# Optimization experiments

Hardware: AMD Instinct MI355X
Metric: run time of the kernel (lower is better)

## Reference

```python
import jax, jax.numpy as jnp
import numpy as np

EPS = 1e-9  # Dice BatchNorm epsilon

def _dice(x, alpha, mm, mv):
    # Keras BN(center=False, scale=False) in inference mode: (x - moving_mean) / sqrt(moving_var + eps)
    p = jax.nn.sigmoid((x - mm) * jax.lax.rsqrt(mv + EPS))
    return x * (p + alpha * (1.0 - p))

def setup_inputs() -> dict:
    key = jax.random.key(0)
    ks = jax.random.split(key, 8)
    B, T, E = 4096, 200, 12
    return {
        "query": jax.random.normal(ks[0], (B, 1, E), jnp.float32),
        "keys": jax.random.normal(ks[1], (B, T, E), jnp.float32),
        "mask": jnp.ones((B, T), dtype=bool),
        "W0": jax.random.normal(ks[2], (48, 80), jnp.float32) * (1.0 / np.sqrt(48)),
        "b0": jnp.zeros((80,), jnp.float32),
        "W1": jax.random.normal(ks[3], (80, 40), jnp.float32) * (1.0 / np.sqrt(80)),
        "b1": jnp.zeros((40,), jnp.float32),
        "alpha0": jax.random.uniform(ks[4], (80,), jnp.float32),
        "alpha1": jax.random.uniform(ks[5], (40,), jnp.float32),
        "mm0": jnp.zeros((80,), jnp.float32),
        "mv0": jnp.ones((80,), jnp.float32),
        "mm1": jnp.zeros((40,), jnp.float32),
        "mv1": jnp.ones((40,), jnp.float32),
        "atten_kernel": jax.random.normal(ks[6], (40, 1), jnp.float32) * (1.0 / np.sqrt(40)),
        "atten_bias": jnp.zeros((1,), jnp.float32),
    }

def reference(query, keys, mask, W0, b0, W1, b1, alpha0, alpha1,
              mm0, mv0, mm1, mv1, atten_kernel, atten_bias):
    B, T, E = keys.shape
    q = jnp.broadcast_to(query, (B, T, E))  # K.repeat_elements(query, T, 1)
    att = jnp.concatenate([q, keys, q - keys, q * keys], axis=-1)  # [B, T, 4E=48]
    h = _dice(jnp.einsum('bti,io->bto', att, W0) + b0, alpha0, mm0, mv0)  # [B,T,80]
    h = _dice(jnp.einsum('bti,io->bto', h, W1) + b1, alpha1, mm1, mv1)    # [B,T,40]
    score = jnp.einsum('bti,io->bto', h, atten_kernel) + atten_bias       # [B,T,1]
    scores = jnp.swapaxes(score, 1, 2)  # [B,1,T]
    # NOTE: original code computes tf.where(mask,...) but overwrites it and
    # matmuls the UNMASKED scores with keys (bug reproduced faithfully).
    return jnp.matmul(scores, keys)  # [B,1,E]
```

## Files before the change

### kernel.cpp

```cpp
#include <hip/hip_runtime.h>
#include <math.h>

#define B_TOT 4096
#define T_LEN 200
#define E_DIM 12
#define LOG2E 1.44269504088896340736f

typedef __attribute__((ext_vector_type(8))) short bf16x8;
typedef __attribute__((ext_vector_type(4))) float f32x4;


__device__ inline unsigned short f2bf(float f) {
    union { float f; unsigned u; } x; x.f = f;
    unsigned r = x.u + 0x7FFFu + ((x.u >> 16) & 1u);
    return (unsigned short)(r >> 16);
}

__global__ __launch_bounds__(256) void din_prep(
    const float* __restrict__ W0, const float* __restrict__ b0v,
    const float* __restrict__ W1, const float* __restrict__ b1v,
    const float* __restrict__ a0, const float* __restrict__ a1,
    const float* __restrict__ mm0, const float* __restrict__ mv0,
    const float* __restrict__ mm1, const float* __restrict__ mv1,
    const float* __restrict__ ak, void* __restrict__ wsv)
{
    unsigned char* wsb = (unsigned char*)wsv;
    unsigned short* w0e = (unsigned short*)wsb;
    unsigned short* w1e = (unsigned short*)(wsb + 10240);
    float* d0c = (float*)(wsb + 19456);
    float* d1c = (float*)(wsb + 20736);

    int idx = blockIdx.x * 256 + threadIdx.x;
    if (idx < 5120) {
        int n = idx >> 6, k = idx & 63;
        float v;
        if (k < 12)        v = W0[(12 + k) * 80 + n] - W0[(24 + k) * 80 + n];
        else if (k < 24)   v = W0[(36 + (k - 12)) * 80 + n];
        else if (k < 36)   v = W0[(k - 24) * 80 + n] + W0[(24 + (k - 24)) * 80 + n];
        else if (k == 36)  v = b0v[n];
        else               v = 0.0f;
        w0e[n * 64 + k] = f2bf(v);
    } else if (idx < 9728) {
        int v2 = idx - 5120;
        int n = v2 / 96, k = v2 - n * 96;
        float v = 0.0f;
        if (n < 40) {
            if (k < 80)       v = W1[k * 40 + n];
            else if (k == 80) v = b1v[n];
        }
        w1e[n * 96 + k] = f2bf(v);
    } else if (idx < 10048) {
        int v2 = idx - 9728;
        int o = v2 >> 2, c = v2 & 3;
        float rs = rsqrtf(mv0[o] + 1e-9f) * LOG2E;
        float val = (c == 0) ? -rs : (c == 1) ? mm0[o] * rs : (c == 2) ? a0[o] : 1.0f - a0[o];
        d0c[o * 4 + c] = val;
    } else {
        int v2 = idx - 10048;
        int j = v2 >> 2, c = v2 & 3;
        float val = 0.0f;
        if (j < 40) {
            float rs = rsqrtf(mv1[j] + 1e-9f) * LOG2E;
            val = (c == 0) ? -rs : (c == 1) ? mm1[j] * rs : (c == 2) ? a1[j] * ak[j]
                                                          : (1.0f - a1[j]) * ak[j];
        }
        d1c[j * 4 + c] = val;
    }
}

#define A0_STRIDE 72
#define H_STRIDE  104

__global__ __launch_bounds__(256, 2) void din_mfma(
    const float* __restrict__ query, const float* __restrict__ keys,
    const float* __restrict__ abias_p, const void* __restrict__ wsv,
    float* __restrict__ out)
{
    __shared__ __align__(16) unsigned short Aseg[4 * 64];
    __shared__ __align__(16) unsigned short A0[4 * 64 * A0_STRIDE];
    __shared__ __align__(16) unsigned short H[4 * 16 * H_STRIDE];

    const unsigned char* wsb = (const unsigned char*)wsv;
    const unsigned short* w0e = (const unsigned short*)wsb;
    const unsigned short* w1e = (const unsigned short*)(wsb + 10240);
    const f32x4* d0cp = (const f32x4*)(wsb + 19456);
    const f32x4* d1cp = (const f32x4*)(wsb + 20736);

    const int tid = threadIdx.x;
    const int lane = tid & 63;
    const int w = tid >> 6;
    const int l15 = lane & 15;
    const int quad = lane >> 4;
    const int b = blockIdx.x * 4 + w;

    unsigned short* A0w = &A0[w * 64 * A0_STRIDE];
    unsigned short* Hw  = &H[w * 16 * H_STRIDE];
    unsigned short* Asw = &Aseg[w * 64];

    bf16x8 b0f[5][2];
    #pragma unroll
    for (int nt = 0; nt < 5; ++nt)
        #pragma unroll
        for (int ks = 0; ks < 2; ++ks)
            b0f[nt][ks] = *(const bf16x8*)(w0e + (nt * 16 + l15) * 64 + ks * 32 + quad * 8);
    bf16x8 b1f[3][3];
    #pragma unroll
    for (int nt = 0; nt < 3; ++nt)
        #pragma unroll
        for (int ks = 0; ks < 3; ++ks)
            b1f[nt][ks] = *(const bf16x8*)(w1e + (nt * 16 + l15) * 96 + ks * 32 + quad * 8);
    f32x4 d0c[5];
    #pragma unroll
    for (int nt = 0; nt < 5; ++nt) d0c[nt] = d0cp[nt * 16 + l15];
    f32x4 d1c[3];
    #pragma unroll
    for (int nt = 0; nt < 3; ++nt) d1c[nt] = d1cp[nt * 16 + l15];
    const float abias = abias_p[0];

    float qq[12];
    {
        const float4* qp = (const float4*)(query + (size_t)b * E_DIM);
        float4 q0 = qp[0], q1 = qp[1], q2 = qp[2];
        qq[0]=q0.x; qq[1]=q0.y; qq[2]=q0.z; qq[3]=q0.w;
        qq[4]=q1.x; qq[5]=q1.y; qq[6]=q1.z; qq[7]=q1.w;
        qq[8]=q2.x; qq[9]=q2.y; qq[10]=q2.z; qq[11]=q2.w;
    }
    unsigned qqw[6];
    #pragma unroll
    for (int i = 0; i < 6; ++i)
        qqw[i] = (unsigned)f2bf(qq[2 * i]) | ((unsigned)f2bf(qq[2 * i + 1]) << 16);

    if (quad == 0) {
        bf16x8 one8 = {(short)0x3F80, 0, 0, 0, 0, 0, 0, 0};
        bf16x8 zero8 = {0, 0, 0, 0, 0, 0, 0, 0};
        *(bf16x8*)(Hw + l15 * H_STRIDE + 80) = one8;
        *(bf16x8*)(Hw + l15 * H_STRIDE + 88) = zero8;
    }

    f32x4 acc2 = {0.f, 0.f, 0.f, 0.f};

    for (int c = 0; c < 4; ++c) {
        const int t0 = c * 64;
        const int myT = t0 + lane;
        const bool valid = myT < T_LEN;

        float kk[12];
        if (valid) {
            const float4* kp = (const float4*)(keys + ((size_t)b * T_LEN + myT) * E_DIM);
            float4 k0 = kp[0], k1 = kp[1], k2 = kp[2];
            kk[0]=k0.x; kk[1]=k0.y; kk[2]=k0.z; kk[3]=k0.w;
            kk[4]=k1.x; kk[5]=k1.y; kk[6]=k1.z; kk[7]=k1.w;
            kk[8]=k2.x; kk[9]=k2.y; kk[10]=k2.z; kk[11]=k2.w;
        } else {
            #pragma unroll
            for (int i = 0; i < 12; ++i) kk[i] = 0.0f;
        }
        {
            unsigned wds[32];
            #pragma unroll
            for (int i = 0; i < 6; ++i)
                wds[i] = (unsigned)f2bf(kk[2 * i]) | ((unsigned)f2bf(kk[2 * i + 1]) << 16);
            #pragma unroll
            for (int i = 0; i < 6; ++i)
                wds[6 + i] = (unsigned)f2bf(qq[2 * i] * kk[2 * i])
                           | ((unsigned)f2bf(qq[2 * i + 1] * kk[2 * i + 1]) << 16);
            #pragma unroll
            for (int i = 0; i < 6; ++i) wds[12 + i] = qqw[i];
            wds[18] = 0x00003F80u;
            #pragma unroll
            for (int i = 19; i < 32; ++i) wds[i] = 0u;
            unsigned short* dst = A0w + lane * A0_STRIDE;
            #pragma unroll
            for (int v = 0; v < 8; ++v) {
                bf16x8 pk;
                #pragma unroll
                for (int h = 0; h < 4; ++h) {
                    unsigned u = wds[v * 4 + h];
                    pk[2 * h]     = (short)(u & 0xFFFF);
                    pk[2 * h + 1] = (short)(u >> 16);
                }
                *(bf16x8*)(dst + v * 8) = pk;
            }
        }
        Asw[lane] = 0;

        const int ntiles = (c < 3) ? 4 : 1;
        for (int ti = 0; ti < ntiles; ++ti) {
            const unsigned short* ar = A0w + (ti * 16 + l15) * A0_STRIDE + quad * 8;
            bf16x8 a0 = *(const bf16x8*)ar;
            bf16x8 a1 = *(const bf16x8*)(ar + 32);

            f32x4 acc[5];
            #pragma unroll
            for (int nt = 0; nt < 5; ++nt) {
                f32x4 cc = {0.f, 0.f, 0.f, 0.f};
                cc = __builtin_amdgcn_mfma_f32_16x16x32_bf16(a0, b0f[nt][0], cc, 0, 0, 0);
                cc = __builtin_amdgcn_mfma_f32_16x16x32_bf16(a1, b0f[nt][1], cc, 0, 0, 0);
                acc[nt] = cc;
            }
            #pragma unroll
            for (int nt = 0; nt < 5; ++nt) {
                #pragma unroll
                for (int r = 0; r < 4; ++r) {
                    float z = acc[nt][r];
                    float pg = __builtin_amdgcn_rcpf(
                        1.0f + __builtin_amdgcn_exp2f(fmaf(z, d0c[nt].x, d0c[nt].y)));
                    float h = z * fmaf(pg, d0c[nt].w, d0c[nt].z);
                    Hw[(quad * 4 + r) * H_STRIDE + nt * 16 + l15] = f2bf(h);
                }
            }
            bf16x8 af[3];
            #pragma unroll
            for (int ks = 0; ks < 3; ++ks)
                af[ks] = *(const bf16x8*)(Hw + l15 * H_STRIDE + ks * 32 + quad * 8);
            float s[4] = {0.f, 0.f, 0.f, 0.f};
            #pragma unroll
            for (int nt = 0; nt < 3; ++nt) {
                f32x4 cc = {0.f, 0.f, 0.f, 0.f};
                #pragma unroll
                for (int ks = 0; ks < 3; ++ks)
                    cc = __builtin_amdgcn_mfma_f32_16x16x32_bf16(af[ks], b1f[nt][ks], cc, 0, 0, 0);
                #pragma unroll
                for (int r = 0; r < 4; ++r) {
                    float z = cc[r];
                    float pg = __builtin_amdgcn_rcpf(
                        1.0f + __builtin_amdgcn_exp2f(fmaf(z, d1c[nt].x, d1c[nt].y)));
                    s[r] = fmaf(z, fmaf(pg, d1c[nt].w, d1c[nt].z), s[r]);
                }
            }
            #pragma unroll
            for (int m = 1; m < 16; m <<= 1) {
                #pragma unroll
                for (int r = 0; r < 4; ++r) s[r] += __shfl_xor(s[r], m, 64);
            }
            if (l15 == 0) {
                unsigned long long pk = 0ull;
                #pragma unroll
                for (int r = 0; r < 4; ++r) {
                    int t = t0 + ti * 16 + quad * 4 + r;
                    unsigned short sb = (t < T_LEN) ? f2bf(s[r] + abias) : (unsigned short)0;
                    pk |= (unsigned long long)sb << (16 * r);
                }
                *(unsigned long long*)(Asw + ti * 16 + quad * 4) = pk;
            }
        }

        #pragma unroll
        for (int ks = 0; ks < 2; ++ks) {
            bf16x8 pa = *(const bf16x8*)(Asw + l15 * 64 + ks * 32 + quad * 8);
            bf16x8 bk;
            #pragma unroll
            for (int j = 0; j < 8; ++j)
                bk[j] = (short)A0w[(ks * 32 + quad * 8 + j) * A0_STRIDE + l15];
            acc2 = __builtin_amdgcn_mfma_f32_16x16x32_bf16(pa, bk, acc2, 0, 0, 0);
        }
    }

    if (quad == 0 && l15 < 12)
        out[(size_t)b * E_DIM + l15] = acc2[0];
}

extern "C" void kernel_launch(void* const* d_in, const int* in_sizes, int n_in,
                              void* d_out, int out_size, void* d_ws, size_t ws_size,
                              hipStream_t stream) {
    const float* query = (const float*)d_in[0];
    const float* keys  = (const float*)d_in[1];
    const float* W0  = (const float*)d_in[3];
    const float* b0v = (const float*)d_in[4];
    const float* W1  = (const float*)d_in[5];
    const float* b1v = (const float*)d_in[6];
    const float* a0  = (const float*)d_in[7];
    const float* a1  = (const float*)d_in[8];
    const float* mm0 = (const float*)d_in[9];
    const float* mv0 = (const float*)d_in[10];
    const float* mm1 = (const float*)d_in[11];
    const float* mv1 = (const float*)d_in[12];
    const float* ak  = (const float*)d_in[13];
    const float* ab  = (const float*)d_in[14];
    float* out = (float*)d_out;

    hipLaunchKernelGGL(din_prep, dim3(40), dim3(256), 0, stream,
                       W0, b0v, W1, b1v, a0, a1, mm0, mv0, mm1, mv1, ak, d_ws);
    hipLaunchKernelGGL(din_mfma, dim3(B_TOT / 4), dim3(256), 0, stream,
                       query, keys, ab, d_ws, out);
}
```

Baseline: 155.9 us.

## Hoist per-batch query terms out of layer-0 GEMM and raise occupancy

The query-only part of the first layer (q·(W0a+W0c) plus bias) is computed once per batch row with one MFMA per output tile and added as a per-column offset. This halves the K dimension of the per-token layer-0 GEMM from 64 to 32 and shrinks the A0 LDS tile. W1 fragments and Dice constants are now reloaded from global/cache inside the loop rather than held in registers, and launch bounds move to 4 blocks per CU for higher occupancy. The trade is more memory traffic for weights against fewer VGPRs and MFMAs.

```diff
diff --git a/kernel.cpp b/kernel.cpp
--- a/kernel.cpp
+++ b/kernel.cpp
@@ -1,4 +1,5 @@
 #include <hip/hip_runtime.h>
+#include <hip/hip_bf16.h>
 #include <math.h>
 
 #define B_TOT 4096
@@ -8,12 +9,19 @@
 
 typedef __attribute__((ext_vector_type(8))) short bf16x8;
 typedef __attribute__((ext_vector_type(4))) float f32x4;
+typedef unsigned short ushort_t;
 
 
 __device__ inline unsigned short f2bf(float f) {
     union { float f; unsigned u; } x; x.f = f;
     unsigned r = x.u + 0x7FFFu + ((x.u >> 16) & 1u);
     return (unsigned short)(r >> 16);
+}
+__device__ inline unsigned pk_bf16(float a, float b) {
+    float2 t; t.x = a; t.y = b;
+    __hip_bfloat162 h = __float22bfloat162_rn(t);
+    union { __hip_bfloat162 h; unsigned u; } cv; cv.h = h;
+    return cv.u;
 }
 
 __global__ __launch_bounds__(256) void din_prep(
@@ -25,21 +33,26 @@
     const float* __restrict__ ak, void* __restrict__ wsv)
 {
     unsigned char* wsb = (unsigned char*)wsv;
-    unsigned short* w0e = (unsigned short*)wsb;
-    unsigned short* w1e = (unsigned short*)(wsb + 10240);
+    ushort_t* w0e2 = (ushort_t*)wsb;
+    ushort_t* wq   = (ushort_t*)(wsb + 5120);
+    ushort_t* w1e  = (ushort_t*)(wsb + 10240);
     float* d0c = (float*)(wsb + 19456);
     float* d1c = (float*)(wsb + 20736);
 
     int idx = blockIdx.x * 256 + threadIdx.x;
-    if (idx < 5120) {
-        int n = idx >> 6, k = idx & 63;
-        float v;
-        if (k < 12)        v = W0[(12 + k) * 80 + n] - W0[(24 + k) * 80 + n];
-        else if (k < 24)   v = W0[(36 + (k - 12)) * 80 + n];
-        else if (k < 36)   v = W0[(k - 24) * 80 + n] + W0[(24 + (k - 24)) * 80 + n];
-        else if (k == 36)  v = b0v[n];
-        else               v = 0.0f;
-        w0e[n * 64 + k] = f2bf(v);
+    if (idx < 2560) {
+        int n = idx >> 5, k = idx & 31;
+        float v = 0.0f;
+        if (k < 12)       v = W0[(12 + k) * 80 + n] - W0[(24 + k) * 80 + n];
+        else if (k < 24)  v = W0[(36 + (k - 12)) * 80 + n];
+        w0e2[n * 32 + k] = f2bf(v);
+    } else if (idx < 5120) {
+        int v2 = idx - 2560;
+        int n = v2 >> 5, k = v2 & 31;
+        float v = 0.0f;
+        if (k < 12)       v = W0[k * 80 + n] + W0[(24 + k) * 80 + n];
+        else if (k == 12) v = b0v[n];
+        wq[n * 32 + k] = f2bf(v);
     } else if (idx < 9728) {
         int v2 = idx - 5120;
         int n = v2 / 96, k = v2 - n * 96;
@@ -68,21 +81,21 @@
     }
 }
 
-#define A0_STRIDE 72
-#define H_STRIDE  104
-
-__global__ __launch_bounds__(256, 2) void din_mfma(
+#define A0_STR 40
+#define H_STR  104
+
+__global__ __launch_bounds__(256, 4) void din_mfma(
     const float* __restrict__ query, const float* __restrict__ keys,
     const float* __restrict__ abias_p, const void* __restrict__ wsv,
     float* __restrict__ out)
 {
-    __shared__ __align__(16) unsigned short Aseg[4 * 64];
-    __shared__ __align__(16) unsigned short A0[4 * 64 * A0_STRIDE];
-    __shared__ __align__(16) unsigned short H[4 * 16 * H_STRIDE];
-
+    __shared__ __align__(16) ushort_t Aseg[4 * 64];
+    __shared__ __align__(16) ushort_t A0[4 * 64 * A0_STR];
+    __shared__ __align__(16) ushort_t H[4 * 16 * H_STR];
     const unsigned char* wsb = (const unsigned char*)wsv;
-    const unsigned short* w0e = (const unsigned short*)wsb;
-    const unsigned short* w1e = (const unsigned short*)(wsb + 10240);
+    const ushort_t* w0e2 = (const ushort_t*)wsb;
+    const ushort_t* wq   = (const ushort_t*)(wsb + 5120);
+    const ushort_t* w1e  = (const ushort_t*)(wsb + 10240);
     const f32x4* d0cp = (const f32x4*)(wsb + 19456);
     const f32x4* d1cp = (const f32x4*)(wsb + 20736);
 
@@ -93,29 +106,14 @@
     const int quad = lane >> 4;
     const int b = blockIdx.x * 4 + w;
 
-    unsigned short* A0w = &A0[w * 64 * A0_STRIDE];
-    unsigned short* Hw  = &H[w * 16 * H_STRIDE];
-    unsigned short* Asw = &Aseg[w * 64];
-
-    bf16x8 b0f[5][2];
+    ushort_t* A0w = &A0[w * 64 * A0_STR];
+    ushort_t* Hw  = &H[w * 16 * H_STR];
+    ushort_t* Asw = &Aseg[w * 64];
+
+    bf16x8 b0f[5];
     #pragma unroll
     for (int nt = 0; nt < 5; ++nt)
-        #pragma unroll
-        for (int ks = 0; ks < 2; ++ks)
-            b0f[nt][ks] = *(const bf16x8*)(w0e + (nt * 16 + l15) * 64 + ks * 32 + quad * 8);
-    bf16x8 b1f[3][3];
-    #pragma unroll
-    for (int nt = 0; nt < 3; ++nt)
-        #pragma unroll
-        for (int ks = 0; ks < 3; ++ks)
-            b1f[nt][ks] = *(const bf16x8*)(w1e + (nt * 16 + l15) * 96 + ks * 32 + quad * 8);
-    f32x4 d0c[5];
-    #pragma unroll
-    for (int nt = 0; nt < 5; ++nt) d0c[nt] = d0cp[nt * 16 + l15];
-    f32x4 d1c[3];
-    #pragma unroll
-    for (int nt = 0; nt < 3; ++nt) d1c[nt] = d1cp[nt * 16 + l15];
-    const float abias = abias_p[0];
+        b0f[nt] = *(const bf16x8*)(w0e2 + (nt * 16 + l15) * 32 + quad * 8);
 
     float qq[12];
     {
@@ -125,16 +123,34 @@
         qq[4]=q1.x; qq[5]=q1.y; qq[6]=q1.z; qq[7]=q1.w;
         qq[8]=q2.x; qq[9]=q2.y; qq[10]=q2.z; qq[11]=q2.w;
     }
-    unsigned qqw[6];
-    #pragma unroll
-    for (int i = 0; i < 6; ++i)
-        qqw[i] = (unsigned)f2bf(qq[2 * i]) | ((unsigned)f2bf(qq[2 * i + 1]) << 16);
+
+    float z0q[5];
+    {
+        unsigned dw0, dw1, dw2, dw3;
+        unsigned p01 = pk_bf16(qq[0], qq[1]), p23 = pk_bf16(qq[2], qq[3]);
+        unsigned p45 = pk_bf16(qq[4], qq[5]), p67 = pk_bf16(qq[6], qq[7]);
+        unsigned p89 = pk_bf16(qq[8], qq[9]), pab = pk_bf16(qq[10], qq[11]);
+        dw0 = (quad == 0) ? p01 : (quad == 1) ? p89 : 0u;
+        dw1 = (quad == 0) ? p23 : (quad == 1) ? pab : 0u;
+        dw2 = (quad == 0) ? p45 : (quad == 1) ? 0x00003F80u : 0u;
+        dw3 = (quad == 0) ? p67 : 0u;
+        union { unsigned u[4]; bf16x8 v; } qa;
+        qa.u[0] = dw0; qa.u[1] = dw1; qa.u[2] = dw2; qa.u[3] = dw3;
+        #pragma unroll
+        for (int nt = 0; nt < 5; ++nt) {
+            bf16x8 wf = *(const bf16x8*)(wq + (nt * 16 + l15) * 32 + quad * 8);
+            f32x4 zz = {0.f, 0.f, 0.f, 0.f};
+            zz = __builtin_amdgcn_mfma_f32_16x16x32_bf16(qa.v, wf, zz, 0, 0, 0);
+            z0q[nt] = zz[0];
+        }
+    }
+    const float abias = abias_p[0];
 
     if (quad == 0) {
         bf16x8 one8 = {(short)0x3F80, 0, 0, 0, 0, 0, 0, 0};
         bf16x8 zero8 = {0, 0, 0, 0, 0, 0, 0, 0};
-        *(bf16x8*)(Hw + l15 * H_STRIDE + 80) = one8;
-        *(bf16x8*)(Hw + l15 * H_STRIDE + 88) = zero8;
+        *(bf16x8*)(Hw + l15 * H_STR + 80) = one8;
+        *(bf16x8*)(Hw + l15 * H_STR + 88) = zero8;
     }
 
     f32x4 acc2 = {0.f, 0.f, 0.f, 0.f};
@@ -156,76 +172,64 @@
             for (int i = 0; i < 12; ++i) kk[i] = 0.0f;
         }
         {
-            unsigned wds[32];
+            unsigned kw[6], qkw[6];
             #pragma unroll
             for (int i = 0; i < 6; ++i)
-                wds[i] = (unsigned)f2bf(kk[2 * i]) | ((unsigned)f2bf(kk[2 * i + 1]) << 16);
+                kw[i] = pk_bf16(kk[2 * i], kk[2 * i + 1]);
             #pragma unroll
             for (int i = 0; i < 6; ++i)
-                wds[6 + i] = (unsigned)f2bf(qq[2 * i] * kk[2 * i])
-                           | ((unsigned)f2bf(qq[2 * i + 1] * kk[2 * i + 1]) << 16);
-            #pragma unroll
-            for (int i = 0; i < 6; ++i) wds[12 + i] = qqw[i];
-            wds[18] = 0x00003F80u;
-            #pragma unroll
-            for (int i = 19; i < 32; ++i) wds[i] = 0u;
-            unsigned short* dst = A0w + lane * A0_STRIDE;
-            #pragma unroll
-            for (int v = 0; v < 8; ++v) {
-                bf16x8 pk;
-                #pragma unroll
-                for (int h = 0; h < 4; ++h) {
-                    unsigned u = wds[v * 4 + h];
-                    pk[2 * h]     = (short)(u & 0xFFFF);
-                    pk[2 * h + 1] = (short)(u >> 16);
-                }
-                *(bf16x8*)(dst + v * 8) = pk;
-            }
+                qkw[i] = pk_bf16(qq[2 * i] * kk[2 * i], qq[2 * i + 1] * kk[2 * i + 1]);
+            uint4* dst = (uint4*)(A0w + lane * A0_STR);
+            uint4 v0, v1, v2, v3;
+            v0.x = kw[0];  v0.y = kw[1];  v0.z = kw[2];  v0.w = kw[3];
+            v1.x = kw[4];  v1.y = kw[5];  v1.z = qkw[0]; v1.w = qkw[1];
+            v2.x = qkw[2]; v2.y = qkw[3]; v2.z = qkw[4]; v2.w = qkw[5];
+            v3.x = 0u;     v3.y = 0u;     v3.z = 0u;     v3.w = 0u;
+            dst[0] = v0; dst[1] = v1; dst[2] = v2; dst[3] = v3;
         }
         Asw[lane] = 0;
 
         const int ntiles = (c < 3) ? 4 : 1;
         for (int ti = 0; ti < ntiles; ++ti) {
-            const unsigned short* ar = A0w + (ti * 16 + l15) * A0_STRIDE + quad * 8;
-            bf16x8 a0 = *(const bf16x8*)ar;
-            bf16x8 a1 = *(const bf16x8*)(ar + 32);
-
+            bf16x8 a0 = *(const bf16x8*)(A0w + (ti * 16 + l15) * A0_STR + quad * 8);
             f32x4 acc[5];
             #pragma unroll
             for (int nt = 0; nt < 5; ++nt) {
                 f32x4 cc = {0.f, 0.f, 0.f, 0.f};
-                cc = __builtin_amdgcn_mfma_f32_16x16x32_bf16(a0, b0f[nt][0], cc, 0, 0, 0);
-                cc = __builtin_amdgcn_mfma_f32_16x16x32_bf16(a1, b0f[nt][1], cc, 0, 0, 0);
-                acc[nt] = cc;
+                acc[nt] = __builtin_amdgcn_mfma_f32_16x16x32_bf16(a0, b0f[nt], cc, 0, 0, 0);
             }
             #pragma unroll
             for (int nt = 0; nt < 5; ++nt) {
+                f32x4 dc = d0cp[nt * 16 + l15];
                 #pragma unroll
                 for (int r = 0; r < 4; ++r) {
-                    float z = acc[nt][r];
+                    float z = acc[nt][r] + z0q[nt];
                     float pg = __builtin_amdgcn_rcpf(
-                        1.0f + __builtin_amdgcn_exp2f(fmaf(z, d0c[nt].x, d0c[nt].y)));
-                    float h = z * fmaf(pg, d0c[nt].w, d0c[nt].z);
-                    Hw[(quad * 4 + r) * H_STRIDE + nt * 16 + l15] = f2bf(h);
+                        1.0f + __builtin_amdgcn_exp2f(fmaf(z, dc.x, dc.y)));
+                    float h = z * fmaf(pg, dc.w, dc.z);
+                    Hw[(quad * 4 + r) * H_STR + nt * 16 + l15] = f2bf(h);
                 }
             }
             bf16x8 af[3];
             #pragma unroll
             for (int ks = 0; ks < 3; ++ks)
-                af[ks] = *(const bf16x8*)(Hw + l15 * H_STRIDE + ks * 32 + quad * 8);
+                af[ks] = *(const bf16x8*)(Hw + l15 * H_STR + ks * 32 + quad * 8);
             float s[4] = {0.f, 0.f, 0.f, 0.f};
             #pragma unroll
             for (int nt = 0; nt < 3; ++nt) {
                 f32x4 cc = {0.f, 0.f, 0.f, 0.f};
                 #pragma unroll
-                for (int ks = 0; ks < 3; ++ks)
-                    cc = __builtin_amdgcn_mfma_f32_16x16x32_bf16(af[ks], b1f[nt][ks], cc, 0, 0, 0);
+                for (int ks = 0; ks < 3; ++ks) {
+                    bf16x8 bf = *(const bf16x8*)(w1e + (nt * 16 + l15) * 96 + ks * 32 + quad * 8);
+                    cc = __builtin_amdgcn_mfma_f32_16x16x32_bf16(af[ks], bf, cc, 0, 0, 0);
+                }
+                f32x4 dc1 = d1cp[nt * 16 + l15];
                 #pragma unroll
                 for (int r = 0; r < 4; ++r) {
                     float z = cc[r];
                     float pg = __builtin_amdgcn_rcpf(
-                        1.0f + __builtin_amdgcn_exp2f(fmaf(z, d1c[nt].x, d1c[nt].y)));
-                    s[r] = fmaf(z, fmaf(pg, d1c[nt].w, d1c[nt].z), s[r]);
+                        1.0f + __builtin_amdgcn_exp2f(fmaf(z, dc1.x, dc1.y)));
+                    s[r] = fmaf(z, fmaf(pg, dc1.w, dc1.z), s[r]);
                 }
             }
             #pragma unroll
@@ -251,7 +255,7 @@
             bf16x8 bk;
             #pragma unroll
             for (int j = 0; j < 8; ++j)
-                bk[j] = (short)A0w[(ks * 32 + quad * 8 + j) * A0_STRIDE + l15];
+                bk[j] = (short)A0w[(ks * 32 + quad * 8 + j) * A0_STR + l15];
             acc2 = __builtin_amdgcn_mfma_f32_16x16x32_bf16(pa, bk, acc2, 0, 0, 0);
         }
     }
```

Measured after the change: 170.8 us. +9.6%, slower.
